# Kernel tuning notes

Hardware: AMD Instinct MI355X
Metric: run time of the kernel (lower is better)

Reference implementation:

```python
import jax, jax.numpy as jnp
import numpy as np

DIM = 1024
N_HEADS = 16
HEAD_DIM = DIM // N_HEADS
B, T = 2, 2048


def get_rotary_embedding(T, head_dim, dtype=jnp.float32):
    inv_freq = 1.0 / (10000.0 ** (jnp.arange(0, head_dim, 2, dtype=jnp.float32) / head_dim))
    t = jnp.arange(T, dtype=jnp.float32)
    freqs = jnp.einsum('t,f->tf', t, inv_freq)          # [T, head_dim/2]
    emb = jnp.concatenate([freqs, freqs], axis=-1)       # [T, head_dim]
    return jnp.sin(emb).astype(dtype), jnp.cos(emb).astype(dtype)


def rotate_half(x):
    x1, x2 = jnp.split(x, 2, axis=-1)
    return jnp.concatenate([-x2, x1], axis=-1)


def apply_rotary_pos_emb(x, sin, cos):
    # x: [B, H, T, D]; sin/cos: [T, D] broadcast over B, H
    return x * cos + rotate_half(x) * sin


def setup_inputs() -> dict:
    key = jax.random.key(0)
    ks = jax.random.split(key, 4)
    s = DIM ** -0.5
    return {
        'x': jax.random.normal(ks[0], (B, T, DIM), jnp.float32),
        'W_qkv': jax.random.normal(ks[1], (DIM, 3 * DIM), jnp.float32) * s,
        'b_qkv': jnp.zeros((3 * DIM,), jnp.float32),
        'W_out': jax.random.normal(ks[2], (DIM, DIM), jnp.float32) * s,
        'b_out': jnp.zeros((DIM,), jnp.float32),
    }


def reference(x, W_qkv, b_qkv, W_out, b_out):
    Bc, Tc, C = x.shape
    scale = HEAD_DIM ** -0.5
    qkv = x @ W_qkv + b_qkv                                    # [B, T, 3C]
    qkv = qkv.reshape(Bc, Tc, 3, N_HEADS, HEAD_DIM)
    qkv = jnp.transpose(qkv, (2, 0, 3, 1, 4))                  # [3, B, H, T, D]
    q, k, v = qkv[0], qkv[1], qkv[2]
    sin, cos = get_rotary_embedding(Tc, HEAD_DIM, x.dtype)
    q = apply_rotary_pos_emb(q, sin, cos)
    k = apply_rotary_pos_emb(k, sin, cos)
    attn = jnp.einsum('bhqd,bhkd->bhqk', q, k) * scale         # [B, H, T, T]
    probs = jax.nn.softmax(attn, axis=-1)
    out = jnp.einsum('bhqk,bhkd->bhqd', probs, v)              # [B, H, T, D]
    out = jnp.transpose(out, (0, 2, 1, 3)).reshape(Bc, Tc, C)
    return out @ W_out + b_out
```

## Files before the change

kernel.cpp:

```cpp
#include <hip/hip_runtime.h>
#include <hip/hip_bf16.h>
#include <cstdint>
#include <cstddef>

typedef unsigned short ushort_t;
typedef __bf16 bf16x8 __attribute__((ext_vector_type(8)));
typedef float f32x4 __attribute__((ext_vector_type(4)));

#define DEV static __device__ __forceinline__

DEV void gl2lds16(const void* g, void* l) {
  __builtin_amdgcn_global_load_lds(
      (const __attribute__((address_space(1))) void*)(uintptr_t)g,
      (__attribute__((address_space(3))) void*)(uintptr_t)l, 16, 0, 0);
}

DEV bf16x8 ldfrag(const void* p) { return __builtin_bit_cast(bf16x8, *(const uint4*)p); }

DEV f32x4 mfma16(bf16x8 a, bf16x8 b, f32x4 c) {
  return __builtin_amdgcn_mfma_f32_16x16x32_bf16(a, b, c, 0, 0, 0);
}

DEV ushort_t f2b(float f) { return __builtin_bit_cast(ushort_t, __float2bfloat16(f)); }
DEV unsigned int pk2(float lo, float hi) {
  return (unsigned int)f2b(lo) | ((unsigned int)f2b(hi) << 16);
}
DEV unsigned int cvtpk(float lo, float hi) {
  unsigned int r;
  asm("v_cvt_pk_bf16_f32 %0, %1, %2" : "=v"(r) : "v"(lo), "v"(hi));
  return r;
}

__global__ __launch_bounds__(256) void k_cast_bf16(const float* __restrict__ X,
                                                   ushort_t* __restrict__ Y, int n) {
  int i = (blockIdx.x * 256 + threadIdx.x) * 4;
  if (i >= n) return;
  float4 v = *(const float4*)(X + i);
  ushort4 o;
  o.x = f2b(v.x); o.y = f2b(v.y); o.z = f2b(v.z); o.w = f2b(v.w);
  *(ushort4*)(Y + i) = o;
}

__global__ __launch_bounds__(256) void k_castT(const float* __restrict__ W,
                                               ushort_t* __restrict__ WT, int K, int N) {
  __shared__ ushort_t tile[64][72];
  int n0 = blockIdx.x * 64, k0 = blockIdx.y * 64;
  int t = threadIdx.x;
#pragma unroll
  for (int i = 0; i < 16; ++i) {
    int e = i * 256 + t; int r = e >> 6, c = e & 63;
    tile[c][r] = f2b(W[(size_t)(k0 + r) * N + n0 + c]);
  }
  __syncthreads();
#pragma unroll
  for (int i = 0; i < 16; ++i) {
    int e = i * 256 + t; int rn = e >> 6, ck = e & 63;
    WT[(size_t)(n0 + rn) * K + k0 + ck] = tile[rn][ck];
  }
}

__global__ __launch_bounds__(256) void k_rope_table(float* __restrict__ sintab,
                                                    float* __restrict__ costab) {
  int id = blockIdx.x * 256 + threadIdx.x;
  int f = id & 31, t = id >> 5;
  float invf = exp2f(-(float)f * 0.4152410118609203f);
  float ang = (float)t * invf;
  sintab[id] = sinf(ang);
  costab[id] = cosf(ang);
}

template <int EPI, int BM, int BN>
__global__ __launch_bounds__(256, 2) void k_gemm_bt(
    const ushort_t* __restrict__ A, const ushort_t* __restrict__ BT,
    const float* __restrict__ bias, ushort_t* __restrict__ Oq,
    ushort_t* __restrict__ Ok, ushort_t* __restrict__ Ov,
    float* __restrict__ Of, const float* __restrict__ sintab,
    const float* __restrict__ costab, int K, int N) {
  constexpr int MI = BM / 32, NJ = BN / 32;
  __shared__ __align__(16) char As[BM * 64];
  __shared__ __align__(16) char Bs[BN * 64];
  const int tid = threadIdx.x, lane = tid & 63, wv = tid >> 6;
  const int l15 = lane & 15, l4 = lane >> 4;
  const int nt = blockIdx.x, mt = blockIdx.y;
  const char* Ab = (const char*)(A + (size_t)mt * BM * K);
  const char* Bb = (const char*)(BT + (size_t)nt * BN * K);
  const int rs = K * 2;
  const int wr = (wv >> 1) * (BM / 2), wc = (wv & 1) * (BN / 2);
  f32x4 acc[MI][NJ] = {};
  for (int k0 = 0; k0 < K; k0 += 32) {
    __syncthreads();
#pragma unroll
    for (int ii = 0; ii < BM / 64; ++ii) {
      int slot = wv * (BM / 64) + ii;
      int r = slot * 16 + (lane >> 2);
      int scb = ((lane & 3) * 16) ^ ((r & 3) << 4);
      gl2lds16(Ab + (size_t)r * rs + k0 * 2 + scb, As + slot * 1024);
    }
#pragma unroll
    for (int ii = 0; ii < BN / 64; ++ii) {
      int slot = wv * (BN / 64) + ii;
      int r = slot * 16 + (lane >> 2);
      int scb = ((lane & 3) * 16) ^ ((r & 3) << 4);
      gl2lds16(Bb + (size_t)r * rs + k0 * 2 + scb, Bs + slot * 1024);
    }
    __syncthreads();
    bf16x8 af[MI], bg[NJ];
#pragma unroll
    for (int i = 0; i < MI; ++i) {
      int r = wr + i * 16 + l15;
      af[i] = ldfrag(As + r * 64 + ((l4 * 16) ^ ((r & 3) << 4)));
    }
#pragma unroll
    for (int j = 0; j < NJ; ++j) {
      int r = wc + j * 16 + l15;
      bg[j] = ldfrag(Bs + r * 64 + ((l4 * 16) ^ ((r & 3) << 4)));
    }
#pragma unroll
    for (int i = 0; i < MI; ++i)
#pragma unroll
      for (int j = 0; j < NJ; ++j)
        acc[i][j] = mfma16(af[i], bg[j], acc[i][j]);
  }
  if constexpr (EPI == 0) {
    const int colbase = nt * BN + wc;
    const int part = colbase >> 10;
    const int h = (colbase >> 6) & 15;
    float bv[NJ];
#pragma unroll
    for (int j = 0; j < NJ; ++j) bv[j] = bias[colbase + j * 16 + l15];
    if (part <= 1) {
      ushort_t* dst = part ? Ok : Oq;
      const float sc = part ? 1.0f : 0.18033688011112042f;
#pragma unroll
      for (int i = 0; i < MI; ++i) {
        int m0 = mt * BM + wr + i * 16 + l4 * 4;
#pragma unroll
        for (int e = 0; e < 4; ++e) {
          int row = m0 + e;
          int bb = row >> 11, t = row & 2047;
          size_t rb = ((size_t)(bb * 16 + h) * 2048 + t) * 64;
#pragma unroll
          for (int j = 0; j < 2; ++j) {
            int f = j * 16 + l15;
            float x1 = acc[i][j][e] + bv[j];
            float x2 = acc[i][j + 2][e] + bv[j + 2];
            float sn = sintab[t * 32 + f], cs = costab[t * 32 + f];
            dst[rb + f]      = f2b((x1 * cs - x2 * sn) * sc);
            dst[rb + f + 32] = f2b((x2 * cs + x1 * sn) * sc);
          }
        }
      }
    } else {
#pragma unroll
      for (int i = 0; i < MI; ++i) {
        int m0 = mt * BM + wr + i * 16 + l4 * 4;
        int bb = m0 >> 11, t0 = m0 & 2047;
#pragma unroll
        for (int j = 0; j < NJ; ++j) {
          int d = j * 16 + l15;
          ushort4 pk;
          pk.x = f2b(acc[i][j][0] + bv[j]);
          pk.y = f2b(acc[i][j][1] + bv[j]);
          pk.z = f2b(acc[i][j][2] + bv[j]);
          pk.w = f2b(acc[i][j][3] + bv[j]);
          *(ushort4*)(Ov + ((size_t)(bb * 16 + h) * 64 + d) * 2048 + t0) = pk;
        }
      }
    }
  } else {
#pragma unroll
    for (int j = 0; j < NJ; ++j) {
      int c = nt * BN + wc + j * 16 + l15;
      float bvv = bias[c];
#pragma unroll
      for (int i = 0; i < MI; ++i) {
        int m0 = mt * BM + wr + i * 16 + l4 * 4;
#pragma unroll
        for (int e = 0; e < 4; ++e)
          Of[(size_t)(m0 + e) * N + c] = acc[i][j][e] + bvv;
      }
    }
  }
}

__global__ __launch_bounds__(256, 2) void k_attn(const ushort_t* __restrict__ Q,
                                                 const ushort_t* __restrict__ K,
                                                 const ushort_t* __restrict__ VT,
                                                 ushort_t* __restrict__ AO) {
  __shared__ __align__(16) char Kt[2][8192];
  __shared__ __align__(16) char Vt[2][8192];
  __shared__ __align__(16) char Pl[4][4608];
  const int tid = threadIdx.x, lane = tid & 63, wv = tid >> 6;
  const int l15 = lane & 15, l4 = lane >> 4;
  const int bh = blockIdx.x, qt = blockIdx.y;
  const int qbase = qt * 128 + wv * 32;

  const char* Qb = (const char*)(Q + ((size_t)bh * 2048 + qbase) * 64);
  bf16x8 bq[2][2];
#pragma unroll
  for (int qh = 0; qh < 2; ++qh)
#pragma unroll
    for (int c = 0; c < 2; ++c)
      bq[qh][c] = ldfrag(Qb + (qh * 16 + l15) * 128 + c * 64 + l4 * 16);

  const char* Kbase = (const char*)(K + (size_t)bh * 2048 * 64);
  const char* Vbase = (const char*)(VT + (size_t)bh * 64 * 2048);
  char* Pw = Pl[wv];

  const int sr = lane >> 3;
  const int scb = ((lane & 7) * 16) ^ ((sr & 7) << 4);

  const f32x4 mInit = {-16.f, -16.f, -16.f, -16.f};
  f32x4 ps4[2] = {};
  f32x4 o[2][4] = {};

#pragma unroll
  for (int ii = 0; ii < 2; ++ii) {
    int slot = wv * 2 + ii;
    int r = slot * 8 + sr;
    gl2lds16(Kbase + (size_t)r * 128 + scb, Kt[0] + slot * 1024);
    gl2lds16(Vbase + (size_t)r * 4096 + scb, Vt[0] + slot * 1024);
  }
  __syncthreads();

  for (int kt = 0; kt < 32; ++kt) {
    const int cur = kt & 1;
    if (kt < 31) {
#pragma unroll
      for (int ii = 0; ii < 2; ++ii) {
        int slot = wv * 2 + ii;
        int r = slot * 8 + sr;
        gl2lds16(Kbase + ((size_t)((kt + 1) * 64 + r)) * 128 + scb, Kt[cur ^ 1] + slot * 1024);
        gl2lds16(Vbase + (size_t)r * 4096 + (kt + 1) * 128 + scb, Vt[cur ^ 1] + slot * 1024);
      }
    }
    const char* Kb = Kt[cur];
    const char* Vb = Vt[cur];
    const int sw = (l15 & 7) << 4;

    f32x4 s[2][4];
    __builtin_amdgcn_s_setprio(1);
#pragma unroll
    for (int j = 0; j < 4; ++j) {
      int r = j * 16 + l15;
      bf16x8 k0 = ldfrag(Kb + r * 128 + ((l4 * 16) ^ sw));
      bf16x8 k1 = ldfrag(Kb + r * 128 + ((64 + l4 * 16) ^ sw));
#pragma unroll
      for (int qh = 0; qh < 2; ++qh) {
        f32x4 z = mfma16(k0, bq[qh][0], mInit);
        s[qh][j] = mfma16(k1, bq[qh][1], z);
      }
    }
    __builtin_amdgcn_s_setprio(0);

#pragma unroll
    for (int qh = 0; qh < 2; ++qh) {
#pragma unroll
      for (int j = 0; j < 4; ++j) {
        f32x4 p;
#pragma unroll
        for (int e = 0; e < 4; ++e) p[e] = exp2f(s[qh][j][e]);
        ps4[qh] += p;
        uint2 w;
        w.x = cvtpk(p[0], p[1]);
        w.y = cvtpk(p[2], p[3]);
        *(uint2*)(Pw + (qh * 16 + l15) * 144 + (j * 16 + l4 * 4) * 2) = w;
      }
    }

    __builtin_amdgcn_s_setprio(1);
#pragma unroll
    for (int c = 0; c < 2; ++c) {
      bf16x8 bp[2];
#pragma unroll
      for (int qh = 0; qh < 2; ++qh)
        bp[qh] = ldfrag(Pw + (qh * 16 + l15) * 144 + c * 64 + l4 * 16);
#pragma unroll
      for (int dt = 0; dt < 4; ++dt) {
        int r = dt * 16 + l15;
        bf16x8 av = ldfrag(Vb + r * 128 + ((c * 64 + l4 * 16) ^ sw));
#pragma unroll
        for (int qh = 0; qh < 2; ++qh) o[qh][dt] = mfma16(av, bp[qh], o[qh][dt]);
      }
    }
    __builtin_amdgcn_s_setprio(0);
    __syncthreads();
  }

  const int b = bh >> 4, h = bh & 15;
#pragma unroll
  for (int qh = 0; qh < 2; ++qh) {
    float t = (ps4[qh][0] + ps4[qh][1]) + (ps4[qh][2] + ps4[qh][3]);
    t += __shfl_xor(t, 16);
    t += __shfl_xor(t, 32);
    float inv = 1.0f / t;
    int q = qbase + qh * 16 + l15;
    ushort_t* dst = AO + ((size_t)(b * 2048 + q)) * 1024 + h * 64;
#pragma unroll
    for (int dt = 0; dt < 4; ++dt) {
      ushort4 pk;
      pk.x = f2b(o[qh][dt][0] * inv);
      pk.y = f2b(o[qh][dt][1] * inv);
      pk.z = f2b(o[qh][dt][2] * inv);
      pk.w = f2b(o[qh][dt][3] * inv);
      *(ushort4*)(dst + dt * 16 + l4 * 4) = pk;
    }
  }
}

extern "C" void kernel_launch(void* const* d_in, const int* in_sizes, int n_in,
                              void* d_out, int out_size, void* d_ws, size_t ws_size,
                              hipStream_t stream) {
  (void)in_sizes; (void)n_in; (void)out_size;
  const float* x    = (const float*)d_in[0];
  const float* Wqkv = (const float*)d_in[1];
  const float* bqkv = (const float*)d_in[2];
  const float* Wout = (const float*)d_in[3];
  const float* bout = (const float*)d_in[4];
  float* out = (float*)d_out;
  char* ws = (char*)d_ws;

  ushort_t* X16 = (ushort_t*)(ws + 0);
  ushort_t* WQT = (ushort_t*)(ws + 8388608);
  ushort_t* WOT = (ushort_t*)(ws + 14680064);
  ushort_t* QB  = (ushort_t*)(ws + 16777216);
  ushort_t* KB  = (ushort_t*)(ws + 25165824);
  ushort_t* VTT = (ushort_t*)(ws + 33554432);
  float* SINT   = (float*)(ws + 41943040);
  float* COST   = SINT + 65536;
  ushort_t* AO  = X16;

  if (ws_size < (size_t)42467328) return;

  k_cast_bf16<<<4096, 256, 0, stream>>>(x, X16, 4194304);
  k_castT<<<dim3(48, 16), 256, 0, stream>>>(Wqkv, WQT, 1024, 3072);
  k_castT<<<dim3(16, 16), 256, 0, stream>>>(Wout, WOT, 1024, 1024);
  k_rope_table<<<256, 256, 0, stream>>>(SINT, COST);
  k_gemm_bt<0, 128, 128><<<dim3(24, 32), 256, 0, stream>>>(
      X16, WQT, bqkv, QB, KB, VTT, nullptr, SINT, COST, 1024, 3072);
  k_attn<<<dim3(32, 16), 256, 0, stream>>>(QB, KB, VTT, AO);
  k_gemm_bt<1, 64, 128><<<dim3(8, 64), 256, 0, stream>>>(
      AO, WOT, bout, nullptr, nullptr, nullptr, out, nullptr, nullptr, 1024, 1024);
}
```

Before: 133.1 us.

## Double-buffer GEMM LDS tiles and swizzle attention P scratch layout

The GEMM kernel now keeps two LDS buffers for the A and B tiles and prefetches the next K-slice while computing on the current one, leaving one barrier per iteration instead of two. MFMA issue is given raised wave priority. In the attention kernel the per-wave P staging buffer drops its padded 144-byte row stride for a 128-byte stride with an XOR swizzle, which shrinks LDS use while still aiming to avoid bank conflicts. The extra GEMM LDS could lower occupancy, and the swizzle only works if `sw` suits the P row indexing.

Measured after the change: 130.6 us. Within noise of the previous version (-1.9%).

```diff
diff --git a/kernel.cpp b/kernel.cpp
--- a/kernel.cpp
+++ b/kernel.cpp
@@ -22,9 +22,6 @@
 }
 
 DEV ushort_t f2b(float f) { return __builtin_bit_cast(ushort_t, __float2bfloat16(f)); }
-DEV unsigned int pk2(float lo, float hi) {
-  return (unsigned int)f2b(lo) | ((unsigned int)f2b(hi) << 16);
-}
 DEV unsigned int cvtpk(float lo, float hi) {
   unsigned int r;
   asm("v_cvt_pk_bf16_f32 %0, %1, %2" : "=v"(r) : "v"(lo), "v"(hi));
@@ -77,8 +74,8 @@
     float* __restrict__ Of, const float* __restrict__ sintab,
     const float* __restrict__ costab, int K, int N) {
   constexpr int MI = BM / 32, NJ = BN / 32;
-  __shared__ __align__(16) char As[BM * 64];
-  __shared__ __align__(16) char Bs[BN * 64];
+  __shared__ __align__(16) char As[2][BM * 64];
+  __shared__ __align__(16) char Bs[2][BN * 64];
   const int tid = threadIdx.x, lane = tid & 63, wv = tid >> 6;
   const int l15 = lane & 15, l4 = lane >> 4;
   const int nt = blockIdx.x, mt = blockIdx.y;
@@ -87,39 +84,58 @@
   const int rs = K * 2;
   const int wr = (wv >> 1) * (BM / 2), wc = (wv & 1) * (BN / 2);
   f32x4 acc[MI][NJ] = {};
+#pragma unroll
+  for (int ii = 0; ii < BM / 64; ++ii) {
+    int slot = wv * (BM / 64) + ii;
+    int r = slot * 16 + (lane >> 2);
+    int scb = ((lane & 3) * 16) ^ ((r & 3) << 4);
+    gl2lds16(Ab + (size_t)r * rs + scb, As[0] + slot * 1024);
+  }
+#pragma unroll
+  for (int ii = 0; ii < BN / 64; ++ii) {
+    int slot = wv * (BN / 64) + ii;
+    int r = slot * 16 + (lane >> 2);
+    int scb = ((lane & 3) * 16) ^ ((r & 3) << 4);
+    gl2lds16(Bb + (size_t)r * rs + scb, Bs[0] + slot * 1024);
+  }
+  __syncthreads();
   for (int k0 = 0; k0 < K; k0 += 32) {
-    __syncthreads();
-#pragma unroll
-    for (int ii = 0; ii < BM / 64; ++ii) {
-      int slot = wv * (BM / 64) + ii;
-      int r = slot * 16 + (lane >> 2);
-      int scb = ((lane & 3) * 16) ^ ((r & 3) << 4);
-      gl2lds16(Ab + (size_t)r * rs + k0 * 2 + scb, As + slot * 1024);
-    }
-#pragma unroll
-    for (int ii = 0; ii < BN / 64; ++ii) {
-      int slot = wv * (BN / 64) + ii;
-      int r = slot * 16 + (lane >> 2);
-      int scb = ((lane & 3) * 16) ^ ((r & 3) << 4);
-      gl2lds16(Bb + (size_t)r * rs + k0 * 2 + scb, Bs + slot * 1024);
-    }
-    __syncthreads();
+    const int cur = (k0 >> 5) & 1;
+    if (k0 + 32 < K) {
+#pragma unroll
+      for (int ii = 0; ii < BM / 64; ++ii) {
+        int slot = wv * (BM / 64) + ii;
+        int r = slot * 16 + (lane >> 2);
+        int scb = ((lane & 3) * 16) ^ ((r & 3) << 4);
+        gl2lds16(Ab + (size_t)r * rs + (k0 + 32) * 2 + scb, As[cur ^ 1] + slot * 1024);
+      }
+#pragma unroll
+      for (int ii = 0; ii < BN / 64; ++ii) {
+        int slot = wv * (BN / 64) + ii;
+        int r = slot * 16 + (lane >> 2);
+        int scb = ((lane & 3) * 16) ^ ((r & 3) << 4);
+        gl2lds16(Bb + (size_t)r * rs + (k0 + 32) * 2 + scb, Bs[cur ^ 1] + slot * 1024);
+      }
+    }
     bf16x8 af[MI], bg[NJ];
 #pragma unroll
     for (int i = 0; i < MI; ++i) {
       int r = wr + i * 16 + l15;
-      af[i] = ldfrag(As + r * 64 + ((l4 * 16) ^ ((r & 3) << 4)));
+      af[i] = ldfrag(As[cur] + r * 64 + ((l4 * 16) ^ ((r & 3) << 4)));
     }
 #pragma unroll
     for (int j = 0; j < NJ; ++j) {
       int r = wc + j * 16 + l15;
-      bg[j] = ldfrag(Bs + r * 64 + ((l4 * 16) ^ ((r & 3) << 4)));
-    }
+      bg[j] = ldfrag(Bs[cur] + r * 64 + ((l4 * 16) ^ ((r & 3) << 4)));
+    }
+    __builtin_amdgcn_s_setprio(1);
 #pragma unroll
     for (int i = 0; i < MI; ++i)
 #pragma unroll
       for (int j = 0; j < NJ; ++j)
         acc[i][j] = mfma16(af[i], bg[j], acc[i][j]);
+    __builtin_amdgcn_s_setprio(0);
+    __syncthreads();
   }
   if constexpr (EPI == 0) {
     const int colbase = nt * BN + wc;
@@ -189,7 +205,7 @@
                                                  ushort_t* __restrict__ AO) {
   __shared__ __align__(16) char Kt[2][8192];
   __shared__ __align__(16) char Vt[2][8192];
-  __shared__ __align__(16) char Pl[4][4608];
+  __shared__ __align__(16) char Pl[4][4096];
   const int tid = threadIdx.x, lane = tid & 63, wv = tid >> 6;
   const int l15 = lane & 15, l4 = lane >> 4;
   const int bh = blockIdx.x, qt = blockIdx.y;
@@ -264,7 +280,7 @@
         uint2 w;
         w.x = cvtpk(p[0], p[1]);
         w.y = cvtpk(p[2], p[3]);
-        *(uint2*)(Pw + (qh * 16 + l15) * 144 + (j * 16 + l4 * 4) * 2) = w;
+        *(uint2*)(Pw + (qh * 16 + l15) * 128 + ((j * 32 + l4 * 8) ^ sw)) = w;
       }
     }
 
@@ -274,7 +290,7 @@
       bf16x8 bp[2];
 #pragma unroll
       for (int qh = 0; qh < 2; ++qh)
-        bp[qh] = ldfrag(Pw + (qh * 16 + l15) * 144 + c * 64 + l4 * 16);
+        bp[qh] = ldfrag(Pw + (qh * 16 + l15) * 128 + ((c * 64 + l4 * 16) ^ sw));
 #pragma unroll
       for (int dt = 0; dt < 4; ++dt) {
         int r = dt * 16 + l15;
```
